# Performance work log

Measured on AMD Instinct MI355X. Metric: run time of the kernel, lower is better.

Reference implementation:

```python
import jax, jax.numpy as jnp
import numpy as np

D_MODEL = 256
N_HEADS = 8
N_LEVELS = 4
N_POINTS = 4
D_FFN = 1024
HW = 128
LQ = HW * HW
LIN = N_LEVELS * LQ
BATCH = 2
HEAD_DIM = D_MODEL // N_HEADS
SPATIAL = [(HW, HW)] * N_LEVELS  # static (H, W) per level
EPS = 1e-5


def _layer_norm(x, g, b):
    m = jnp.mean(x, axis=-1, keepdims=True)
    v = jnp.mean(jnp.square(x - m), axis=-1, keepdims=True)
    return (x - m) * jax.lax.rsqrt(v + EPS) * g + b


def _gather(v, idx):
    # v: (N, heads, HW, hd); idx: (N, heads, Lq, P) -> (N, heads, Lq, P, hd)
    N, Hh, Lq, P = idx.shape
    out = jnp.take_along_axis(v, idx.reshape(N, Hh, Lq * P)[..., None], axis=2)
    return out.reshape(N, Hh, Lq, P, -1)


def _ms_deform_attn_core(value, loc, attn):
    # value: (N, Lin, heads, hd); loc: (N, Lq, heads, L, P, 2) in [0,1]; attn: (N, Lq, heads, L, P)
    N, _, Hh, hd = value.shape
    Lq = loc.shape[1]
    out = jnp.zeros((N, Hh, Lq, hd), value.dtype)
    start = 0
    for l, (H, W) in enumerate(SPATIAL):
        v = value[:, start:start + H * W].transpose(0, 2, 1, 3)  # (N, heads, H*W, hd)
        start += H * W
        ll = loc[:, :, :, l].transpose(0, 2, 1, 3, 4)  # (N, heads, Lq, P, 2)
        # F.grid_sample(align_corners=False, padding_mode='zeros') on grid 2*loc-1:
        # pixel coord = loc * size - 0.5
        x = ll[..., 0] * W - 0.5
        y = ll[..., 1] * H - 0.5
        x0 = jnp.floor(x)
        y0 = jnp.floor(y)
        wx = x - x0
        wy = y - y0
        x0i = x0.astype(jnp.int32)
        y0i = y0.astype(jnp.int32)
        acc = jnp.zeros((N, Hh, Lq, N_POINTS, hd), value.dtype)
        for dy, wyc in ((0, 1.0 - wy), (1, wy)):
            for dx, wxc in ((0, 1.0 - wx), (1, wx)):
                xi = x0i + dx
                yi = y0i + dy
                valid = (xi >= 0) & (xi < W) & (yi >= 0) & (yi < H)
                idx = jnp.clip(yi, 0, H - 1) * W + jnp.clip(xi, 0, W - 1)
                g = _gather(v, idx)
                w = (wxc * wyc * valid).astype(value.dtype)
                acc = acc + g * w[..., None]
        aw = attn[:, :, :, l].transpose(0, 2, 1, 3)  # (N, heads, Lq, P)
        out = out + jnp.sum(acc * aw[..., None], axis=3)
    return out.transpose(0, 2, 1, 3).reshape(N, Lq, Hh * hd)


def _forward(cur_src, src_all, pos, reference_points, spatial_shape,
             W_off, b_off, W_attn, b_attn, W_val, b_val, W_out, b_out,
             gamma1, beta1, W1, b1, W2, b2, gamma2, beta2):
    N, Lq, d = cur_src.shape
    q = cur_src + pos[:, -1]                      # with_pos_embed(cur_src, pos[-1])
    inp = src_all + pos.reshape(N, -1, d)         # with_pos_embed(src_all, cat(pos, 1))
    value = (inp @ W_val + b_val).reshape(N, -1, N_HEADS, HEAD_DIM)
    off = (q @ W_off + b_off).reshape(N, Lq, N_HEADS, N_LEVELS, N_POINTS, 2)
    attn = (q @ W_attn + b_attn).reshape(N, Lq, N_HEADS, N_LEVELS * N_POINTS)
    attn = jax.nn.softmax(attn, axis=-1).reshape(N, Lq, N_HEADS, N_LEVELS, N_POINTS)
    # offset_normalizer = stack([W, H], -1)
    normalizer = jnp.stack([spatial_shape[..., 1], spatial_shape[..., 0]], -1).astype(cur_src.dtype)
    loc = reference_points[:, :, None, :, None, :] + off / normalizer[None, None, None, :, None, :]
    src2 = _ms_deform_attn_core(value, loc, attn) @ W_out + b_out
    src = _layer_norm(cur_src + src2, gamma1, beta1)   # dropout is identity in eval
    ffn = jax.nn.relu(src @ W1 + b1) @ W2 + b2
    return _layer_norm(src + ffn, gamma2, beta2)


def setup_inputs():
    key = jax.random.key(0)
    ks = jax.random.split(key, 16)
    s = 0.02
    f32 = jnp.float32
    return {
        "cur_src": jax.random.normal(ks[0], (BATCH, LQ, D_MODEL), f32),
        "src_all": jax.random.normal(ks[1], (BATCH, LIN, D_MODEL), f32),
        "pos": jax.random.normal(ks[2], (BATCH, N_LEVELS, LQ, D_MODEL), f32),
        "reference_points": jax.random.uniform(ks[3], (BATCH, LQ, N_LEVELS, 2), f32),
        "spatial_shape": jnp.array(SPATIAL, dtype=jnp.int32),
        "level_start_index": (jnp.arange(N_LEVELS) * LQ).astype(jnp.int32),
        "W_off": jax.random.normal(ks[4], (D_MODEL, N_HEADS * N_LEVELS * N_POINTS * 2), f32) * s,
        "b_off": jax.random.normal(ks[5], (N_HEADS * N_LEVELS * N_POINTS * 2,), f32) * 0.5,
        "W_attn": jax.random.normal(ks[6], (D_MODEL, N_HEADS * N_LEVELS * N_POINTS), f32) * s,
        "b_attn": jnp.zeros((N_HEADS * N_LEVELS * N_POINTS,), f32),
        "W_val": jax.random.normal(ks[7], (D_MODEL, D_MODEL), f32) * s,
        "b_val": jnp.zeros((D_MODEL,), f32),
        "W_out": jax.random.normal(ks[8], (D_MODEL, D_MODEL), f32) * s,
        "b_out": jnp.zeros((D_MODEL,), f32),
        "gamma1": jnp.ones((D_MODEL,), f32),
        "beta1": jnp.zeros((D_MODEL,), f32),
        "W1": jax.random.normal(ks[9], (D_MODEL, D_FFN), f32) * s,
        "b1": jnp.zeros((D_FFN,), f32),
        "W2": jax.random.normal(ks[10], (D_FFN, D_MODEL), f32) * s,
        "b2": jnp.zeros((D_MODEL,), f32),
        "gamma2": jnp.ones((D_MODEL,), f32),
        "beta2": jnp.zeros((D_MODEL,), f32),
    }


def reference(cur_src, src_all, pos, reference_points, spatial_shape, level_start_index,
              W_off, b_off, W_attn, b_attn, W_val, b_val, W_out, b_out,
              gamma1, beta1, W1, b1, W2, b2, gamma2, beta2):
    return _forward(cur_src, src_all, pos, reference_points, spatial_shape,
                    W_off, b_off, W_attn, b_attn, W_val, b_val, W_out, b_out,
                    gamma1, beta1, W1, b1, W2, b2, gamma2, beta2)
```

## Files before the change

kernel.cpp:

```cpp
#include <hip/hip_runtime.h>

#define LQN   16384
#define LINN  65536

typedef __attribute__((ext_vector_type(8))) short bf16x8;
typedef __attribute__((ext_vector_type(4))) float f32x4;
typedef __attribute__((ext_vector_type(4))) unsigned short bf16x4;

__device__ __forceinline__ unsigned short f2bf(float f) {
  unsigned u = __float_as_uint(f);
  u += 0x7FFFu + ((u >> 16) & 1u);
  return (unsigned short)(u >> 16);
}

__global__ __launch_bounds__(256) void wtrans6_kernel(
    const float* __restrict__ Wv, const float* __restrict__ Wo,
    const float* __restrict__ Wa, const float* __restrict__ Wu,
    const float* __restrict__ W1, const float* __restrict__ W2,
    unsigned short* __restrict__ wt) {
  int idx = blockIdx.x * 256 + threadIdx.x;
  const float* W; int K, N, base;
  if (idx < 131072) {
    if (idx < 65536) { W = Wv; K = 256; N = 256; base = 0; }
    else             { W = Wo; K = 256; N = 256; base = 65536; }
  } else if (idx < 229376) {
    if (idx < 163840) { W = Wa; K = 256; N = 128; base = 131072; }
    else              { W = Wu; K = 256; N = 256; base = 163840; }
  } else if (idx < 491520) { W = W1; K = 256; N = 1024; base = 229376; }
  else                     { W = W2; K = 1024; N = 256; base = 491520; }
  int local = idx - base;
  int n = local / K, k = local - n * K;
  wt[idx] = f2bf(W[(size_t)k * N + n]);
}

__global__ __launch_bounds__(256) void q_kernel(const float* __restrict__ cur,
                                                const float* __restrict__ pos,
                                                unsigned short* __restrict__ q) {
  size_t i = (size_t)blockIdx.x * 256 + threadIdx.x;
  size_t row = i >> 6;
  int n = (int)(row >> 14), lq = (int)(row & 16383);
  float4 a = ((const float4*)cur)[i];
  float4 b = ((const float4*)pos)[(((size_t)n * 4 + 3) * LQN + lq) * 64 + (i & 63)];
  bf16x4 o;
  o.x = f2bf(a.x + b.x); o.y = f2bf(a.y + b.y);
  o.z = f2bf(a.z + b.z); o.w = f2bf(a.w + b.w);
  ((bf16x4*)q)[i] = o;
}

template <int A_BF16, int HAS_A2, int DO_RELU, int OUT_BF16>
__global__ __launch_bounds__(256) void gemm_kernel(
    const void* __restrict__ Ap, const float* __restrict__ A2,
    const unsigned short* __restrict__ Bt, const float* __restrict__ bias,
    void* __restrict__ Cp, int M, int N, int K) {
  __shared__ unsigned short As[128][72];
  __shared__ unsigned short Bs[128][72];
  const int tid = threadIdx.x;
  const int m0 = blockIdx.x * 128, n0 = blockIdx.y * 128;
  const int wave = tid >> 6, lane = tid & 63;
  const int wm = (wave >> 1) * 64, wn = (wave & 1) * 64;
  const int l15 = lane & 15, quad = lane >> 4;

  f32x4 acc[4][4];
#pragma unroll
  for (int i = 0; i < 4; i++)
#pragma unroll
    for (int j = 0; j < 4; j++)
#pragma unroll
      for (int r = 0; r < 4; r++) acc[i][j][r] = 0.f;

  for (int k0 = 0; k0 < K; k0 += 64) {
    if (A_BF16) {
      const unsigned short* A = (const unsigned short*)Ap;
      bf16x8 va[4], vb[4];
#pragma unroll
      for (int j = 0; j < 4; j++) {
        int c = tid + j * 256;
        int row = c >> 3, ks = (c & 7) * 8;
        va[j] = *(const bf16x8*)(A + (size_t)(m0 + row) * K + k0 + ks);
      }
#pragma unroll
      for (int j = 0; j < 4; j++) {
        int c = tid + j * 256;
        int row = c >> 3, ks = (c & 7) * 8;
        vb[j] = *(const bf16x8*)(Bt + (size_t)(n0 + row) * K + k0 + ks);
      }
#pragma unroll
      for (int j = 0; j < 4; j++) {
        int c = tid + j * 256;
        int row = c >> 3, ks = (c & 7) * 8;
        *(bf16x8*)&As[row][ks] = va[j];
      }
#pragma unroll
      for (int j = 0; j < 4; j++) {
        int c = tid + j * 256;
        int row = c >> 3, ks = (c & 7) * 8;
        *(bf16x8*)&Bs[row][ks] = vb[j];
      }
    } else {
      const float* A = (const float*)Ap;
      float4 va[8], vw[8];
      bf16x8 vb[4];
#pragma unroll
      for (int j = 0; j < 8; j++) {
        int c = tid + j * 256;
        int row = c >> 4, ks = (c & 15) * 4;
        va[j] = *(const float4*)(A + (size_t)(m0 + row) * K + k0 + ks);
      }
      if (HAS_A2) {
#pragma unroll
        for (int j = 0; j < 8; j++) {
          int c = tid + j * 256;
          int row = c >> 4, ks = (c & 15) * 4;
          vw[j] = *(const float4*)(A2 + (size_t)(m0 + row) * K + k0 + ks);
        }
      }
#pragma unroll
      for (int j = 0; j < 4; j++) {
        int c = tid + j * 256;
        int row = c >> 3, ks = (c & 7) * 8;
        vb[j] = *(const bf16x8*)(Bt + (size_t)(n0 + row) * K + k0 + ks);
      }
#pragma unroll
      for (int j = 0; j < 8; j++) {
        int c = tid + j * 256;
        int row = c >> 4, ks = (c & 15) * 4;
        float4 v = va[j];
        if (HAS_A2) {
          v.x += vw[j].x; v.y += vw[j].y; v.z += vw[j].z; v.w += vw[j].w;
        }
        bf16x4 b;
        b.x = f2bf(v.x); b.y = f2bf(v.y); b.z = f2bf(v.z); b.w = f2bf(v.w);
        *(bf16x4*)&As[row][ks] = b;
      }
#pragma unroll
      for (int j = 0; j < 4; j++) {
        int c = tid + j * 256;
        int row = c >> 3, ks = (c & 7) * 8;
        *(bf16x8*)&Bs[row][ks] = vb[j];
      }
    }
    __syncthreads();
#pragma unroll
    for (int kk = 0; kk < 64; kk += 32) {
      bf16x8 af[4], bfr[4];
#pragma unroll
      for (int i = 0; i < 4; i++) af[i] = *(const bf16x8*)&As[wm + i * 16 + l15][kk + quad * 8];
#pragma unroll
      for (int j = 0; j < 4; j++) bfr[j] = *(const bf16x8*)&Bs[wn + j * 16 + l15][kk + quad * 8];
#pragma unroll
      for (int i = 0; i < 4; i++)
#pragma unroll
        for (int j = 0; j < 4; j++)
          acc[i][j] = __builtin_amdgcn_mfma_f32_16x16x32_bf16(af[i], bfr[j], acc[i][j], 0, 0, 0);
    }
    __syncthreads();
  }
#pragma unroll
  for (int i = 0; i < 4; i++) {
#pragma unroll
    for (int j = 0; j < 4; j++) {
      const int col = n0 + wn + j * 16 + l15;
      const float bv = bias[col];
#pragma unroll
      for (int r = 0; r < 4; r++) {
        const int row = m0 + wm + i * 16 + quad * 4 + r;
        float v = acc[i][j][r] + bv;
        if (DO_RELU) v = fmaxf(v, 0.f);
        if (OUT_BF16)
          ((unsigned short*)Cp)[(size_t)row * N + col] = f2bf(v);
        else
          ((float*)Cp)[(size_t)row * N + col] = v;
      }
    }
  }
}

__global__ __launch_bounds__(256) void sample_kernel(
    const unsigned short* __restrict__ value, const float* __restrict__ offs,
    const float* __restrict__ attnl, const float* __restrict__ refp,
    unsigned int* __restrict__ attn_out) {
  const int tid = threadIdx.x;
  const int sub = tid >> 4;
  const int c = tid & 15;
  const int g = blockIdx.x * 16 + sub;
  const int n = g >> 17;
  const int nl = g >> 3;
  const int h = g & 7;

  const float* lg = attnl + (size_t)nl * 128 + h * 16;
  float e[16];
  float mx = -1e30f;
#pragma unroll
  for (int i = 0; i < 16; i++) { e[i] = lg[i]; mx = fmaxf(mx, e[i]); }
  float s = 0.f;
#pragma unroll
  for (int i = 0; i < 16; i++) { e[i] = __expf(e[i] - mx); s += e[i]; }
  const float inv = 1.f / s;

  const int pt = c;
  const int pl = pt >> 2;
  const float ox = offs[((size_t)g * 16 + pt) * 2 + 0];
  const float oy = offs[((size_t)g * 16 + pt) * 2 + 1];
  const float rx = refp[((size_t)nl * 4 + pl) * 2 + 0];
  const float ry = refp[((size_t)nl * 4 + pl) * 2 + 1];
  const float x = fmaf(rx, 128.f, ox - 0.5f);
  const float y = fmaf(ry, 128.f, oy - 0.5f);
  const float xf = floorf(x), yf = floorf(y);
  const float fx = x - xf, fy = y - yf;
  const int x0 = (int)xf, y0 = (int)yf;
  const float aw = e[pt] * inv;
  const int xc0 = min(max(x0, 0), 127), xc1 = min(max(x0 + 1, 0), 127);
  const int yc0 = min(max(y0, 0), 127), yc1 = min(max(y0 + 1, 0), 127);
  float wx0 = (x0 >= 0 && x0 <= 127) ? (1.f - fx) : 0.f;
  float wx1 = (x0 >= -1 && x0 <= 126) ? fx : 0.f;
  float wy0 = ((y0 >= 0 && y0 <= 127) ? (1.f - fy) : 0.f) * aw;
  float wy1 = ((y0 >= -1 && y0 <= 126) ? fy : 0.f) * aw;
  const int packed = xc0 | (xc1 << 7) | (yc0 << 14) | (yc1 << 21);

  const unsigned int* base0 =
      (const unsigned int*)value + (((size_t)n * LINN) * 8 + h) * 16 + c;

  float a0 = 0.f, a1 = 0.f;
#pragma unroll
  for (int p = 0; p < 16; p++) {
    const int pk = __shfl(packed, p, 16);
    const float w_x0 = __shfl(wx0, p, 16);
    const float w_x1 = __shfl(wx1, p, 16);
    const float w_y0 = __shfl(wy0, p, 16);
    const float w_y1 = __shfl(wy1, p, 16);
    const unsigned int* bl = base0 + (size_t)(p >> 2) * (LQN * 128);
    const int X0 = pk & 127, X1 = (pk >> 7) & 127;
    const int Y0 = (pk >> 14) & 127, Y1 = (pk >> 21) & 127;
    const unsigned v00 = bl[(Y0 * 128 + X0) * 128];
    const unsigned v01 = bl[(Y0 * 128 + X1) * 128];
    const unsigned v10 = bl[(Y1 * 128 + X0) * 128];
    const unsigned v11 = bl[(Y1 * 128 + X1) * 128];
    const float w00 = w_x0 * w_y0, w01 = w_x1 * w_y0;
    const float w10 = w_x0 * w_y1, w11 = w_x1 * w_y1;
    a0 = fmaf(w00, __uint_as_float(v00 << 16), a0);
    a1 = fmaf(w00, __uint_as_float(v00 & 0xFFFF0000u), a1);
    a0 = fmaf(w01, __uint_as_float(v01 << 16), a0);
    a1 = fmaf(w01, __uint_as_float(v01 & 0xFFFF0000u), a1);
    a0 = fmaf(w10, __uint_as_float(v10 << 16), a0);
    a1 = fmaf(w10, __uint_as_float(v10 & 0xFFFF0000u), a1);
    a0 = fmaf(w11, __uint_as_float(v11 << 16), a0);
    a1 = fmaf(w11, __uint_as_float(v11 & 0xFFFF0000u), a1);
  }
  attn_out[(size_t)g * 16 + c] = (unsigned)f2bf(a0) | ((unsigned)f2bf(a1) << 16);
}

template <int EMIT_BF16>
__global__ __launch_bounds__(256) void ln_kernel(const float* __restrict__ x1,
                                                 const float* __restrict__ x2,
                                                 const float* __restrict__ gamma,
                                                 const float* __restrict__ beta,
                                                 float* __restrict__ out,
                                                 unsigned short* __restrict__ outb) {
  const int row = blockIdx.x * 4 + (threadIdx.x >> 6);
  const int lane = threadIdx.x & 63;
  float4 a = ((const float4*)(x1 + (size_t)row * 256))[lane];
  float4 b = ((const float4*)(x2 + (size_t)row * 256))[lane];
  float v0 = a.x + b.x, v1 = a.y + b.y, v2 = a.z + b.z, v3 = a.w + b.w;
  float s1 = v0 + v1 + v2 + v3;
  float s2 = v0 * v0 + v1 * v1 + v2 * v2 + v3 * v3;
#pragma unroll
  for (int o = 1; o < 64; o <<= 1) { s1 += __shfl_xor(s1, o); s2 += __shfl_xor(s2, o); }
  const float mean = s1 * (1.f / 256.f);
  const float var = s2 * (1.f / 256.f) - mean * mean;
  const float rstd = rsqrtf(var + 1e-5f);
  float4 gm = ((const float4*)gamma)[lane];
  float4 bt = ((const float4*)beta)[lane];
  float4 o4;
  o4.x = (v0 - mean) * rstd * gm.x + bt.x;
  o4.y = (v1 - mean) * rstd * gm.y + bt.y;
  o4.z = (v2 - mean) * rstd * gm.z + bt.z;
  o4.w = (v3 - mean) * rstd * gm.w + bt.w;
  ((float4*)(out + (size_t)row * 256))[lane] = o4;
  if (EMIT_BF16) {
    bf16x4 ob;
    ob.x = f2bf(o4.x); ob.y = f2bf(o4.y); ob.z = f2bf(o4.z); ob.w = f2bf(o4.w);
    ((bf16x4*)(outb + (size_t)row * 256))[lane] = ob;
  }
}

extern "C" void kernel_launch(void* const* d_in, const int* in_sizes, int n_in,
                              void* d_out, int out_size, void* d_ws, size_t ws_size,
                              hipStream_t stream) {
  (void)in_sizes; (void)n_in; (void)out_size; (void)ws_size;
  const float* cur_src = (const float*)d_in[0];
  const float* src_all = (const float*)d_in[1];
  const float* pos     = (const float*)d_in[2];
  const float* refp    = (const float*)d_in[3];
  const float* W_off   = (const float*)d_in[6];
  const float* b_off   = (const float*)d_in[7];
  const float* W_attn  = (const float*)d_in[8];
  const float* b_attn  = (const float*)d_in[9];
  const float* W_val   = (const float*)d_in[10];
  const float* b_val   = (const float*)d_in[11];
  const float* W_out   = (const float*)d_in[12];
  const float* b_out   = (const float*)d_in[13];
  const float* gamma1  = (const float*)d_in[14];
  const float* beta1   = (const float*)d_in[15];
  const float* W1      = (const float*)d_in[16];
  const float* b1      = (const float*)d_in[17];
  const float* W2      = (const float*)d_in[18];
  const float* b2      = (const float*)d_in[19];
  const float* gamma2  = (const float*)d_in[20];
  const float* beta2   = (const float*)d_in[21];
  float* out = (float*)d_out;

  char* ws = (char*)d_ws;
  unsigned short* value = (unsigned short*)(ws + 0);
  unsigned short* qbuf  = (unsigned short*)(ws + 67108864);
  float* offbuf         = (float*)(ws + 83886080);
  float* attnl          = (float*)(ws + 117440512);
  unsigned short* attno = (unsigned short*)(ws + 134217728);
  float* src2           = (float*)(ws + 150994944);
  float* srcb           = (float*)(ws + 184549376);
  unsigned short* wt    = (unsigned short*)(ws + 218103808);
  unsigned short* wt_val  = wt;
  unsigned short* wt_off  = wt + 65536;
  unsigned short* wt_attn = wt + 131072;
  unsigned short* wt_out  = wt + 163840;
  unsigned short* wt_1    = wt + 229376;
  unsigned short* wt_2    = wt + 491520;
  unsigned short* srcb_bf = (unsigned short*)attnl;

  wtrans6_kernel<<<2944, 256, 0, stream>>>(W_val, W_off, W_attn, W_out, W1, W2, wt);

  q_kernel<<<8192, 256, 0, stream>>>(cur_src, pos, qbuf);

  gemm_kernel<0, 1, 0, 1><<<dim3(1024, 2), 256, 0, stream>>>(
      src_all, pos, wt_val, b_val, value, 131072, 256, 256);
  gemm_kernel<1, 0, 0, 0><<<dim3(256, 2), 256, 0, stream>>>(
      qbuf, nullptr, wt_off, b_off, offbuf, 32768, 256, 256);
  gemm_kernel<1, 0, 0, 0><<<dim3(256, 1), 256, 0, stream>>>(
      qbuf, nullptr, wt_attn, b_attn, attnl, 32768, 128, 256);
  sample_kernel<<<16384, 256, 0, stream>>>(value, offbuf, attnl, refp,
                                           (unsigned int*)attno);
  gemm_kernel<1, 0, 0, 0><<<dim3(256, 2), 256, 0, stream>>>(
      attno, nullptr, wt_out, b_out, src2, 32768, 256, 256);
  ln_kernel<1><<<8192, 256, 0, stream>>>(cur_src, src2, gamma1, beta1, srcb, srcb_bf);
  gemm_kernel<1, 0, 1, 1><<<dim3(256, 8), 256, 0, stream>>>(
      srcb_bf, nullptr, wt_1, b1, value, 32768, 1024, 256);
  gemm_kernel<1, 0, 0, 0><<<dim3(256, 2), 256, 0, stream>>>(
      value, nullptr, wt_2, b2, offbuf, 32768, 256, 1024);
  ln_kernel<0><<<8192, 256, 0, stream>>>(srcb, offbuf, gamma2, beta2, out, nullptr);
}
```

Measured before the change: 684.5 us.

## Use direct global-to-LDS loads with XOR swizzle in GEMM, merge offset/attn GEMMs

Rewrites the GEMM so global loads go straight into LDS via global_load_lds, using an XOR-swizzled unpadded layout to avoid bank conflicts. The fp32 value-projection input is now pre-added and converted to bf16 in a separate elementwise kernel, fused with the query add. The offset and attention-logit projections become one GEMM with N=384 that splits its output into two buffers. Blocks are linearised with column-fastest order for A-tile reuse. The extra pass writing a bf16 copy of src_all+pos adds memory traffic, and the GEMM loop is still unpipelined.

```diff
diff --git a/kernel.cpp b/kernel.cpp
--- a/kernel.cpp
+++ b/kernel.cpp
@@ -33,32 +33,48 @@
   wt[idx] = f2bf(W[(size_t)k * N + n]);
 }
 
-__global__ __launch_bounds__(256) void q_kernel(const float* __restrict__ cur,
-                                                const float* __restrict__ pos,
-                                                unsigned short* __restrict__ q) {
+__global__ __launch_bounds__(256) void addcvt_kernel(
+    const float* __restrict__ src_all, const float* __restrict__ pos,
+    const float* __restrict__ cur, unsigned short* __restrict__ inp_bf,
+    unsigned short* __restrict__ qb) {
   size_t i = (size_t)blockIdx.x * 256 + threadIdx.x;
-  size_t row = i >> 6;
-  int n = (int)(row >> 14), lq = (int)(row & 16383);
-  float4 a = ((const float4*)cur)[i];
-  float4 b = ((const float4*)pos)[(((size_t)n * 4 + 3) * LQN + lq) * 64 + (i & 63)];
-  bf16x4 o;
-  o.x = f2bf(a.x + b.x); o.y = f2bf(a.y + b.y);
-  o.z = f2bf(a.z + b.z); o.w = f2bf(a.w + b.w);
-  ((bf16x4*)q)[i] = o;
-}
-
-template <int A_BF16, int HAS_A2, int DO_RELU, int OUT_BF16>
-__global__ __launch_bounds__(256) void gemm_kernel(
-    const void* __restrict__ Ap, const float* __restrict__ A2,
-    const unsigned short* __restrict__ Bt, const float* __restrict__ bias,
-    void* __restrict__ Cp, int M, int N, int K) {
-  __shared__ unsigned short As[128][72];
-  __shared__ unsigned short Bs[128][72];
+  if (i < 8388608) {
+    float4 a = ((const float4*)src_all)[i];
+    float4 b = ((const float4*)pos)[i];
+    bf16x4 o;
+    o.x = f2bf(a.x + b.x); o.y = f2bf(a.y + b.y);
+    o.z = f2bf(a.z + b.z); o.w = f2bf(a.w + b.w);
+    ((bf16x4*)inp_bf)[i] = o;
+  } else {
+    size_t j = i - 8388608;
+    size_t row = j >> 6;
+    int n = (int)(row >> 14), lq = (int)(row & 16383);
+    float4 a = ((const float4*)cur)[j];
+    float4 b = ((const float4*)pos)[(((size_t)n * 4 + 3) * LQN + lq) * 64 + (j & 63)];
+    bf16x4 o;
+    o.x = f2bf(a.x + b.x); o.y = f2bf(a.y + b.y);
+    o.z = f2bf(a.z + b.z); o.w = f2bf(a.w + b.w);
+    ((bf16x4*)qb)[j] = o;
+  }
+}
+
+template <int DO_RELU, int OUT_BF16, int SPLIT>
+__global__ __launch_bounds__(256) void gemm_lds_kernel(
+    const unsigned short* __restrict__ A, const unsigned short* __restrict__ Bt,
+    const float* __restrict__ bias, const float* __restrict__ bias2,
+    void* __restrict__ Cp, float* __restrict__ Cp2,
+    int M, int N, int K, int ny) {
+  __shared__ unsigned short As[128 * 64];
+  __shared__ unsigned short Bs[128 * 64];
+  const int bid = blockIdx.x;
+  const int by = bid % ny, bx = bid / ny;
+  const int m0 = bx * 128, n0 = by * 128;
   const int tid = threadIdx.x;
-  const int m0 = blockIdx.x * 128, n0 = blockIdx.y * 128;
   const int wave = tid >> 6, lane = tid & 63;
   const int wm = (wave >> 1) * 64, wn = (wave & 1) * 64;
   const int l15 = lane & 15, quad = lane >> 4;
+  const int rl = lane >> 3;
+  const int cl = (lane & 7) ^ rl;
 
   f32x4 acc[4][4];
 #pragma unroll
@@ -68,85 +84,36 @@
 #pragma unroll
       for (int r = 0; r < 4; r++) acc[i][j][r] = 0.f;
 
+  const unsigned short* Abase = A + (size_t)m0 * K + cl * 8;
+  const unsigned short* Bbase = Bt + (size_t)n0 * K + cl * 8;
+
   for (int k0 = 0; k0 < K; k0 += 64) {
-    if (A_BF16) {
-      const unsigned short* A = (const unsigned short*)Ap;
-      bf16x8 va[4], vb[4];
-#pragma unroll
-      for (int j = 0; j < 4; j++) {
-        int c = tid + j * 256;
-        int row = c >> 3, ks = (c & 7) * 8;
-        va[j] = *(const bf16x8*)(A + (size_t)(m0 + row) * K + k0 + ks);
-      }
-#pragma unroll
-      for (int j = 0; j < 4; j++) {
-        int c = tid + j * 256;
-        int row = c >> 3, ks = (c & 7) * 8;
-        vb[j] = *(const bf16x8*)(Bt + (size_t)(n0 + row) * K + k0 + ks);
-      }
-#pragma unroll
-      for (int j = 0; j < 4; j++) {
-        int c = tid + j * 256;
-        int row = c >> 3, ks = (c & 7) * 8;
-        *(bf16x8*)&As[row][ks] = va[j];
-      }
-#pragma unroll
-      for (int j = 0; j < 4; j++) {
-        int c = tid + j * 256;
-        int row = c >> 3, ks = (c & 7) * 8;
-        *(bf16x8*)&Bs[row][ks] = vb[j];
-      }
-    } else {
-      const float* A = (const float*)Ap;
-      float4 va[8], vw[8];
-      bf16x8 vb[4];
-#pragma unroll
-      for (int j = 0; j < 8; j++) {
-        int c = tid + j * 256;
-        int row = c >> 4, ks = (c & 15) * 4;
-        va[j] = *(const float4*)(A + (size_t)(m0 + row) * K + k0 + ks);
-      }
-      if (HAS_A2) {
-#pragma unroll
-        for (int j = 0; j < 8; j++) {
-          int c = tid + j * 256;
-          int row = c >> 4, ks = (c & 15) * 4;
-          vw[j] = *(const float4*)(A2 + (size_t)(m0 + row) * K + k0 + ks);
-        }
-      }
-#pragma unroll
-      for (int j = 0; j < 4; j++) {
-        int c = tid + j * 256;
-        int row = c >> 3, ks = (c & 7) * 8;
-        vb[j] = *(const bf16x8*)(Bt + (size_t)(n0 + row) * K + k0 + ks);
-      }
-#pragma unroll
-      for (int j = 0; j < 8; j++) {
-        int c = tid + j * 256;
-        int row = c >> 4, ks = (c & 15) * 4;
-        float4 v = va[j];
-        if (HAS_A2) {
-          v.x += vw[j].x; v.y += vw[j].y; v.z += vw[j].z; v.w += vw[j].w;
-        }
-        bf16x4 b;
-        b.x = f2bf(v.x); b.y = f2bf(v.y); b.z = f2bf(v.z); b.w = f2bf(v.w);
-        *(bf16x4*)&As[row][ks] = b;
-      }
-#pragma unroll
-      for (int j = 0; j < 4; j++) {
-        int c = tid + j * 256;
-        int row = c >> 3, ks = (c & 7) * 8;
-        *(bf16x8*)&Bs[row][ks] = vb[j];
-      }
+#pragma unroll
+    for (int t = 0; t < 4; t++) {
+      const int row = wave * 32 + t * 8 + rl;
+      __builtin_amdgcn_global_load_lds(
+          (const __attribute__((address_space(1))) void*)(Abase + (size_t)row * K + k0),
+          (__attribute__((address_space(3))) void*)(As + (wave * 32 + t * 8) * 64),
+          16, 0, 0);
+      __builtin_amdgcn_global_load_lds(
+          (const __attribute__((address_space(1))) void*)(Bbase + (size_t)row * K + k0),
+          (__attribute__((address_space(3))) void*)(Bs + (wave * 32 + t * 8) * 64),
+          16, 0, 0);
     }
     __syncthreads();
 #pragma unroll
-    for (int kk = 0; kk < 64; kk += 32) {
+    for (int kk = 0; kk < 2; kk++) {
       bf16x8 af[4], bfr[4];
 #pragma unroll
-      for (int i = 0; i < 4; i++) af[i] = *(const bf16x8*)&As[wm + i * 16 + l15][kk + quad * 8];
-#pragma unroll
-      for (int j = 0; j < 4; j++) bfr[j] = *(const bf16x8*)&Bs[wn + j * 16 + l15][kk + quad * 8];
+      for (int i = 0; i < 4; i++) {
+        const int row = wm + i * 16 + l15;
+        af[i] = *(const bf16x8*)&As[row * 64 + (((quad + 4 * kk) ^ (row & 7)) * 8)];
+      }
+#pragma unroll
+      for (int j = 0; j < 4; j++) {
+        const int row = wn + j * 16 + l15;
+        bfr[j] = *(const bf16x8*)&Bs[row * 64 + (((quad + 4 * kk) ^ (row & 7)) * 8)];
+      }
 #pragma unroll
       for (int i = 0; i < 4; i++)
 #pragma unroll
@@ -160,16 +127,22 @@
 #pragma unroll
     for (int j = 0; j < 4; j++) {
       const int col = n0 + wn + j * 16 + l15;
-      const float bv = bias[col];
+      float bv;
+      if (SPLIT) bv = (col < 256) ? bias[col] : bias2[col - 256];
+      else       bv = bias[col];
 #pragma unroll
       for (int r = 0; r < 4; r++) {
         const int row = m0 + wm + i * 16 + quad * 4 + r;
         float v = acc[i][j][r] + bv;
         if (DO_RELU) v = fmaxf(v, 0.f);
-        if (OUT_BF16)
+        if (SPLIT) {
+          if (col < 256) ((float*)Cp)[(size_t)row * 256 + col] = v;
+          else           Cp2[(size_t)row * 128 + (col - 256)] = v;
+        } else if (OUT_BF16) {
           ((unsigned short*)Cp)[(size_t)row * N + col] = f2bf(v);
-        else
+        } else {
           ((float*)Cp)[(size_t)row * N + col] = v;
+        }
       }
     }
   }
@@ -319,31 +292,29 @@
   float* srcb           = (float*)(ws + 184549376);
   unsigned short* wt    = (unsigned short*)(ws + 218103808);
   unsigned short* wt_val  = wt;
-  unsigned short* wt_off  = wt + 65536;
-  unsigned short* wt_attn = wt + 131072;
+  unsigned short* wt_qa   = wt + 65536;
   unsigned short* wt_out  = wt + 163840;
   unsigned short* wt_1    = wt + 229376;
   unsigned short* wt_2    = wt + 491520;
   unsigned short* srcb_bf = (unsigned short*)attnl;
+  unsigned short* inp_bf  = (unsigned short*)src2;
 
   wtrans6_kernel<<<2944, 256, 0, stream>>>(W_val, W_off, W_attn, W_out, W1, W2, wt);
 
-  q_kernel<<<8192, 256, 0, stream>>>(cur_src, pos, qbuf);
-
-  gemm_kernel<0, 1, 0, 1><<<dim3(1024, 2), 256, 0, stream>>>(
-      src_all, pos, wt_val, b_val, value, 131072, 256, 256);
-  gemm_kernel<1, 0, 0, 0><<<dim3(256, 2), 256, 0, stream>>>(
-      qbuf, nullptr, wt_off, b_off, offbuf, 32768, 256, 256);
-  gemm_kernel<1, 0, 0, 0><<<dim3(256, 1), 256, 0, stream>>>(
-      qbuf, nullptr, wt_attn, b_attn, attnl, 32768, 128, 256);
+  addcvt_kernel<<<40960, 256, 0, stream>>>(src_all, pos, cur_src, inp_bf, qbuf);
+
+  gemm_lds_kernel<0, 1, 0><<<2048, 256, 0, stream>>>(
+      inp_bf, wt_val, b_val, nullptr, value, nullptr, 131072, 256, 256, 2);
+  gemm_lds_kernel<0, 0, 1><<<768, 256, 0, stream>>>(
+      qbuf, wt_qa, b_off, b_attn, offbuf, attnl, 32768, 384, 256, 3);
   sample_kernel<<<16384, 256, 0, stream>>>(value, offbuf, attnl, refp,
                                            (unsigned int*)attno);
-  gemm_kernel<1, 0, 0, 0><<<dim3(256, 2), 256, 0, stream>>>(
-      attno, nullptr, wt_out, b_out, src2, 32768, 256, 256);
+  gemm_lds_kernel<0, 0, 0><<<512, 256, 0, stream>>>(
+      attno, wt_out, b_out, nullptr, src2, nullptr, 32768, 256, 256, 2);
   ln_kernel<1><<<8192, 256, 0, stream>>>(cur_src, src2, gamma1, beta1, srcb, srcb_bf);
-  gemm_kernel<1, 0, 1, 1><<<dim3(256, 8), 256, 0, stream>>>(
-      srcb_bf, nullptr, wt_1, b1, value, 32768, 1024, 256);
-  gemm_kernel<1, 0, 0, 0><<<dim3(256, 2), 256, 0, stream>>>(
-      value, nullptr, wt_2, b2, offbuf, 32768, 256, 1024);
+  gemm_lds_kernel<1, 1, 0><<<2048, 256, 0, stream>>>(
+      srcb_bf, wt_1, b1, nullptr, value, nullptr, 32768, 1024, 256, 8);
+  gemm_lds_kernel<0, 0, 0><<<512, 256, 0, stream>>>(
+      value, wt_2, b2, nullptr, offbuf, nullptr, 32768, 256, 1024, 2);
   ln_kernel<0><<<8192, 256, 0, stream>>>(srcb, offbuf, gamma2, beta2, out, nullptr);
 }
```

After: 646.6 us. 1.06x faster.
